# Kernel tuning notes

Measured on AMD Instinct MI355X. Metric: run time of the kernel, lower is better.

Reference implementation:

```python
import jax, jax.numpy as jnp
import numpy as np

N, D, K = 8192, 128, 128  # nodes, feature dim, clusters
E = 262144                # edges per graph


def mish(x):
    return x * jnp.tanh(jax.nn.softplus(x))


def sage(x, src, dst, Wl, bl, Wr):
    # PyG SAGEConv: mean-aggregate source features at targets, then lin_l(agg)+lin_r(x)
    agg = jax.ops.segment_sum(x[src], dst, num_segments=N)            # [N,D]
    cnt = jax.ops.segment_sum(jnp.ones((src.shape[0],), x.dtype), dst, num_segments=N)
    mean = agg / jnp.maximum(cnt, 1.0)[:, None]
    return mean @ Wl + bl + x @ Wr


def dmon(x, adj, W1, b1, W2, b2):
    # DMoNPooling (PyG): MLP -> softmax assignments, pooled feats, 3 losses.
    s = jax.nn.softmax((x @ W1 + b1) @ W2 + b2, axis=-1)              # [N,K]
    out = jax.nn.selu(s.T @ x)                                        # [K,D]
    out_adj = s.T @ adj @ s                                           # [K,K]
    deg = adj.sum(-1, keepdims=True)                                  # [N,1]
    m = deg.sum() / 2
    ca = s.T @ deg                                                    # [K,1]
    normalizer = (ca @ ca.T) / 2 / m
    spectral = -jnp.trace(out_adj - normalizer) / 2 / m
    ss = s.T @ s
    i_norm = jnp.sqrt(jnp.asarray(K, x.dtype))                        # ||I_K||_F
    ortho = jnp.linalg.norm(ss / jnp.linalg.norm(ss) - jnp.eye(K, dtype=x.dtype) / i_norm)
    cluster = jnp.linalg.norm(s.sum(0)) / N * i_norm - 1
    return out, spectral, ortho, cluster


def dense_adj(e):
    adj = jnp.zeros((N, N), jnp.float32)
    return adj.at[e[0], e[1]].add(1.0)


def setup_inputs():
    key = jax.random.key(0)
    ks = jax.random.split(key, 24)
    w = lambda k, shp: jax.random.normal(k, shp, jnp.float32) * 0.05
    inp = {
        'x1': jax.random.normal(ks[0], (N, D), jnp.float32),
        'x2': jax.random.normal(ks[1], (N, D), jnp.float32),
        'e1': jax.random.randint(ks[2], (2, E), 0, N),
        'e2': jax.random.randint(ks[3], (2, E), 0, N),
    }
    names = ['c1', 'c2', 'co', 'c3', 'c4']
    for i, nm in enumerate(names):
        inp[nm + '_Wl'] = w(ks[4 + 3 * i], (D, D))
        inp[nm + '_bl'] = jnp.zeros((D,), jnp.float32)
        inp[nm + '_Wr'] = w(ks[5 + 3 * i], (D, D))
    inp['m_W1'] = w(ks[20], (D, D))
    inp['m_b1'] = jnp.zeros((D,), jnp.float32)
    inp['m_W2'] = w(ks[21], (D, K))
    inp['m_b2'] = jnp.zeros((K,), jnp.float32)
    return inp


def reference(x1, x2, e1, e2,
              c1_Wl, c1_bl, c1_Wr, c2_Wl, c2_bl, c2_Wr,
              co_Wl, co_bl, co_Wr, c3_Wl, c3_bl, c3_Wr,
              c4_Wl, c4_bl, c4_Wr, m_W1, m_b1, m_W2, m_b2):
    s1, d1 = e1[0], e1[1]
    s2, d2 = e2[0], e2[1]
    h1 = mish(sage(x1, s1, d1, c1_Wl, c1_bl, c1_Wr))
    h2 = mish(sage(x2, s2, d2, c2_Wl, c2_bl, c2_Wr))
    co1 = mish(sage(h1, s1, d1, co_Wl, co_bl, co_Wr))
    co2 = mish(sage(h2, s2, d2, co_Wl, co_bl, co_Wr))
    h1 = mish(sage(h1 + co1, s1, d1, c3_Wl, c3_bl, c3_Wr))
    h2 = mish(sage(h2 + co2, s2, d2, c4_Wl, c4_bl, c4_Wr))
    p1, sp1, o1, cl1 = dmon(h1, dense_adj(e1), m_W1, m_b1, m_W2, m_b2)
    p2, sp2, o2, cl2 = dmon(h2, dense_adj(e2), m_W1, m_b1, m_W2, m_b2)
    x = jnp.concatenate([p1, p2], axis=0)[None]  # [1, 2K, D]
    return x, sp1 + o1 + cl1 + sp2 + o2 + cl2
```

## Files before the change

kernel.cpp:

```cpp
#include <hip/hip_runtime.h>
#include <math.h>

#define NN 8192
#define DD 128
#define KK 128
#define EE 262144
#define BCAP 128

typedef _Float16 f16;
typedef __attribute__((ext_vector_type(8))) _Float16 f16x8;
typedef __attribute__((ext_vector_type(4))) _Float16 f16x4;
typedef __attribute__((ext_vector_type(4))) float f32x4;

__device__ __forceinline__ float mishf(float v){
  float e  = __expf(v);
  float t2 = e * (e + 2.f);
  float r  = v * (t2 / (t2 + 2.f));
  return (v > 30.f) ? v : r;
}

__device__ __forceinline__ unsigned char enc_fp8(float f){
  unsigned u = __float_as_uint(f) + 0x00080000u;
  int e8 = (int)(u >> 23) - 120;
  if (e8 >= 1) return (unsigned char)(((unsigned)e8 << 3) | ((u >> 20) & 7u));
  return (unsigned char)(f * 512.f + 0.5f);
}
__device__ __forceinline__ float dec_fp8(unsigned b){
  unsigned e = (b >> 3) & 0xFu;
  return e ? __uint_as_float(((e + 120u) << 23) | ((b & 7u) << 20))
           : (float)(b & 7u) * 0.001953125f;
}

__global__ __launch_bounds__(256) void prep_kernel(
    const float* __restrict__ x0, const float* __restrict__ x1,
    f16* __restrict__ f0, f16* __restrict__ f1,
    const int* __restrict__ eA, const int* __restrict__ eB,
    int* cntA, int* degA, int* cntB, int* degB,
    int* __restrict__ bkA, int* __restrict__ bkB,
    const float* w0, const float* w1, const float* w2, const float* w3,
    const float* w4, const float* w5, const float* w6, const float* w7,
    const float* w8, const float* w9, const float* w10, const float* w11,
    f16* WT){
  int g = blockIdx.y;
  int bx = blockIdx.x;
  int t = threadIdx.x;
  if (bx < 512){
    const float* x = g ? x1 : x0;
    f16* f = g ? f1 : f0;
    int idx = bx * 256 + t;
    const float4* p = (const float4*)&x[idx * 8];
    float4 a = p[0], b = p[1];
    f16x8 o;
    o[0] = (f16)a.x; o[1] = (f16)a.y; o[2] = (f16)a.z; o[3] = (f16)a.w;
    o[4] = (f16)b.x; o[5] = (f16)b.y; o[6] = (f16)b.z; o[7] = (f16)b.w;
    *(f16x8*)&f[idx * 8] = o;
  } else if (bx < 768){
    const int* e  = g ? eB : eA;
    int* cnt = g ? cntB : cntA;
    int* deg = g ? degB : degA;
    int* bk  = g ? bkB  : bkA;
    const int* src = e;
    const int* dst = e + EE;
    for (int i = (bx - 512) * 256 + t; i < EE; i += 65536){
      int d = dst[i], s = src[i];
      int pos = atomicAdd(&cnt[d], 1);
      bk[d * BCAP + pos] = s;
      atomicAdd(&deg[s], 1);
    }
  } else {
    const float* Ws[12] = {w0,w1,w2,w3,w4,w5,w6,w7,w8,w9,w10,w11};
    int widx = (bx - 768) * 2 + g;
    const float* W = Ws[widx];
    f16* O = WT + (size_t)widx * 16384;
    int n = t >> 1, k0 = (t & 1) * 64;
#pragma unroll
    for (int seg = 0; seg < 8; ++seg){
      f16x8 o;
#pragma unroll
      for (int q = 0; q < 8; ++q)
        o[q] = (f16)W[(k0 + seg * 8 + q) * 128 + n];
      *(f16x8*)&O[n * 128 + k0 + seg * 8] = o;
    }
  }
}

template<int DUAL, int ACT, int FUSEADD>
__global__ __launch_bounds__(256) void aggemm(
    const int* __restrict__ cntA, const int* __restrict__ cntB,
    const int* __restrict__ bkA, const int* __restrict__ bkB,
    const f16* __restrict__ FA, const f16* __restrict__ FBg,
    const f16* __restrict__ BA, const f16* __restrict__ BBm,
    const f16* __restrict__ WaT0, const f16* __restrict__ WaT1,
    const f16* __restrict__ WbT0, const f16* __restrict__ WbT1,
    const float* __restrict__ bi0, const float* __restrict__ bi1,
    const f16* __restrict__ ADD0, const f16* __restrict__ ADD1,
    f16* __restrict__ O0, f16* __restrict__ O1){
  int g = blockIdx.y;
  const int* cnt = g ? cntB : cntA;
  const int* bk  = g ? bkB  : bkA;
  const f16* F  = g ? FBg : FA;
  const f16* Bm = g ? BBm : BA;
  const f16* WaT = g ? WaT1 : WaT0;
  const f16* WbT = g ? WbT1 : WbT0;
  const float* bi = g ? bi1 : bi0;
  const f16* ADD = g ? ADD1 : ADD0;
  f16* O = g ? O1 : O0;

  __shared__ f16 AT[32][136];
  int t = threadIdx.x;
  int rowBase = blockIdx.x * 32;

  {
    int r = t >> 3;
    int lane = t & 7;
    int c0 = lane * 16;
    int node = rowBase + r;
    int nc = cnt[node];
    const int* lst = bk + node * BCAP;
    float a[16];
#pragma unroll
    for (int k = 0; k < 16; ++k) a[k] = 0.f;
    int j = 0;
    for (; j + 4 <= nc; j += 4){
      int s0 = lst[j], s1 = lst[j + 1], s2 = lst[j + 2], s3 = lst[j + 3];
      f16x8 u0 = *(const f16x8*)&F[s0 * DD + c0];
      f16x8 u1 = *(const f16x8*)&F[s0 * DD + c0 + 8];
      f16x8 v0 = *(const f16x8*)&F[s1 * DD + c0];
      f16x8 v1 = *(const f16x8*)&F[s1 * DD + c0 + 8];
      f16x8 w0 = *(const f16x8*)&F[s2 * DD + c0];
      f16x8 w1 = *(const f16x8*)&F[s2 * DD + c0 + 8];
      f16x8 y0 = *(const f16x8*)&F[s3 * DD + c0];
      f16x8 y1 = *(const f16x8*)&F[s3 * DD + c0 + 8];
#pragma unroll
      for (int k = 0; k < 8; ++k){
        a[k]     += ((float)u0[k] + (float)v0[k]) + ((float)w0[k] + (float)y0[k]);
        a[k + 8] += ((float)u1[k] + (float)v1[k]) + ((float)w1[k] + (float)y1[k]);
      }
    }
    for (; j < nc; ++j){
      int s = lst[j];
      f16x8 u0 = *(const f16x8*)&F[s * DD + c0];
      f16x8 u1 = *(const f16x8*)&F[s * DD + c0 + 8];
#pragma unroll
      for (int k = 0; k < 8; ++k){ a[k] += (float)u0[k]; a[k + 8] += (float)u1[k]; }
    }
    float inv = 1.f / fmaxf((float)nc, 1.f);
    f16x8 o0, o1;
#pragma unroll
    for (int k = 0; k < 8; ++k){ o0[k] = (f16)(a[k] * inv); o1[k] = (f16)(a[k + 8] * inv); }
    *(f16x8*)&AT[r][c0]     = o0;
    *(f16x8*)&AT[r][c0 + 8] = o1;
  }
  __syncthreads();

  int wave = t >> 6, l = t & 63;
  int lrow = l & 15;
  int lk = (l >> 4) * 8;
  int rt = wave >> 1, nh = wave & 1;
  int rowW = rowBase + rt * 16;

  f32x4 acc[4];
#pragma unroll
  for (int q = 0; q < 4; ++q) acc[q] = (f32x4){0.f, 0.f, 0.f, 0.f};

#pragma unroll
  for (int kc = 0; kc < 4; ++kc){
    int kb = kc * 32 + lk;
    f16x8 a0 = *(const f16x8*)&AT[rt * 16 + lrow][kb];
#pragma unroll
    for (int q = 0; q < 4; ++q){
      int nt = nh * 4 + q;
      f16x8 bw = *(const f16x8*)&WaT[(nt * 16 + lrow) * 128 + kb];
      acc[q] = __builtin_amdgcn_mfma_f32_16x16x32_f16(a0, bw, acc[q], 0, 0, 0);
    }
    if (DUAL){
      f16x8 c0v = *(const f16x8*)&Bm[(rowW + lrow) * 128 + kb];
#pragma unroll
      for (int q = 0; q < 4; ++q){
        int nt = nh * 4 + q;
        f16x8 bw = *(const f16x8*)&WbT[(nt * 16 + lrow) * 128 + kb];
        acc[q] = __builtin_amdgcn_mfma_f32_16x16x32_f16(c0v, bw, acc[q], 0, 0, 0);
      }
    }
  }

  int col16 = l & 15;
  int rgrp = (l >> 4) * 4;
#pragma unroll
  for (int r = 0; r < 4; ++r){
    int row = rowW + rgrp + r;
    float v[4];
#pragma unroll
    for (int q = 0; q < 4; ++q) v[q] = acc[q][r] + bi[(nh * 4 + q) * 16 + col16];
    if (ACT == 1){
#pragma unroll
      for (int q = 0; q < 4; ++q) v[q] = mishf(v[q]);
    }
    if (FUSEADD){
#pragma unroll
      for (int q = 0; q < 4; ++q)
        v[q] += (float)ADD[row * 128 + (nh * 4 + q) * 16 + col16];
    }
#pragma unroll
    for (int q = 0; q < 4; ++q)
      O[row * 128 + (nh * 4 + q) * 16 + col16] = (f16)v[q];
  }
}

__global__ __launch_bounds__(128) void mlp_kernel(
    const f16* __restrict__ H0, const f16* __restrict__ H1,
    const f16* __restrict__ W1T, const f16* __restrict__ W2T,
    const float* __restrict__ b1, const float* __restrict__ b2,
    f16* __restrict__ O0, f16* __restrict__ O1,
    unsigned char* __restrict__ S80, unsigned char* __restrict__ S81){
  int g = blockIdx.y;
  const f16* A = g ? H1 : H0;
  f16* O = g ? O1 : O0;
  unsigned char* S8 = g ? S81 : S80;

  __shared__ f16 T[32][136];
  int t = threadIdx.x;
  int wave = t >> 6, l = t & 63;
  int lrow = l & 15;
  int lk = (l >> 4) * 8;
  int rowBase = blockIdx.x * 32 + wave * 16;
  int col16 = l & 15;
  int rgrp = (l >> 4) * 4;

  f32x4 acc[8];
#pragma unroll
  for (int nt = 0; nt < 8; ++nt) acc[nt] = (f32x4){0.f, 0.f, 0.f, 0.f};
#pragma unroll
  for (int kc = 0; kc < 4; ++kc){
    int kb = kc * 32 + lk;
    f16x8 a0 = *(const f16x8*)&A[(rowBase + lrow) * 128 + kb];
#pragma unroll
    for (int nt = 0; nt < 8; ++nt){
      f16x8 bw = *(const f16x8*)&W1T[(nt * 16 + lrow) * 128 + kb];
      acc[nt] = __builtin_amdgcn_mfma_f32_16x16x32_f16(a0, bw, acc[nt], 0, 0, 0);
    }
  }
#pragma unroll
  for (int r = 0; r < 4; ++r)
#pragma unroll
    for (int nt = 0; nt < 8; ++nt)
      T[wave * 16 + rgrp + r][nt * 16 + col16] = (f16)(acc[nt][r] + b1[nt * 16 + col16]);
  __syncthreads();

  f32x4 acc2[8];
#pragma unroll
  for (int nt = 0; nt < 8; ++nt) acc2[nt] = (f32x4){0.f, 0.f, 0.f, 0.f};
#pragma unroll
  for (int kc = 0; kc < 4; ++kc){
    int kb = kc * 32 + lk;
    f16x8 a0 = *(const f16x8*)&T[wave * 16 + lrow][kb];
#pragma unroll
    for (int nt = 0; nt < 8; ++nt){
      f16x8 bw = *(const f16x8*)&W2T[(nt * 16 + lrow) * 128 + kb];
      acc2[nt] = __builtin_amdgcn_mfma_f32_16x16x32_f16(a0, bw, acc2[nt], 0, 0, 0);
    }
  }

  float bv[8];
#pragma unroll
  for (int nt = 0; nt < 8; ++nt) bv[nt] = b2[nt * 16 + col16];
#pragma unroll
  for (int r = 0; r < 4; ++r){
    int row = rowBase + rgrp + r;
    float v[8];
#pragma unroll
    for (int nt = 0; nt < 8; ++nt) v[nt] = acc2[nt][r] + bv[nt];
    float m = v[0];
#pragma unroll
    for (int nt = 1; nt < 8; ++nt) m = fmaxf(m, v[nt]);
    for (int msk = 1; msk < 16; msk <<= 1) m = fmaxf(m, __shfl_xor(m, msk));
    float sum = 0.f;
#pragma unroll
    for (int nt = 0; nt < 8; ++nt){ v[nt] = __expf(v[nt] - m); sum += v[nt]; }
    for (int msk = 1; msk < 16; msk <<= 1) sum += __shfl_xor(sum, msk);
    float inv = 1.f / sum;
#pragma unroll
    for (int nt = 0; nt < 8; ++nt) v[nt] *= inv;
#pragma unroll
    for (int nt = 0; nt < 8; ++nt){
      O[row * 128 + nt * 16 + col16] = (f16)v[nt];
      S8[row * 128 + nt * 16 + col16] = enc_fp8(v[nt] * 64.f);
    }
  }
}

__global__ __launch_bounds__(256) void transpose_kernel(
    const f16* __restrict__ in0A, const f16* __restrict__ in1A,
    const f16* __restrict__ in0B, const f16* __restrict__ in1B,
    f16* __restrict__ o0A, f16* __restrict__ o1A,
    f16* __restrict__ o0B, f16* __restrict__ o1B,
    const int* __restrict__ dg0, const int* __restrict__ dg1,
    float* col0, float* col1, float* ca0, float* ca1){
  int g = blockIdx.y, z = blockIdx.z;
  const f16* in = z ? (g ? in1B : in0B) : (g ? in1A : in0A);
  f16* outp     = z ? (g ? o1B  : o0B)  : (g ? o1A  : o0A);
  __shared__ f16 T[32][136];
  int t = threadIdx.x;
  int i0 = blockIdx.x * 32;
#pragma unroll
  for (int j = 0; j < 2; ++j){
    int idx = t + j * 256;
    int row = idx >> 4, c8 = (idx & 15) * 8;
    f16x8 v = *(const f16x8*)&in[(i0 + row) * 128 + c8];
#pragma unroll
    for (int q = 0; q < 8; ++q) T[row][c8 + q] = v[q];
  }
  __syncthreads();
  int k = t >> 1, seg = (t & 1) * 16;
  f16x8 oA, oB;
#pragma unroll
  for (int q = 0; q < 8; ++q){ oA[q] = T[seg + q][k]; oB[q] = T[seg + 8 + q][k]; }
  *(f16x8*)&outp[(size_t)k * NN + i0 + seg]     = oA;
  *(f16x8*)&outp[(size_t)k * NN + i0 + seg + 8] = oB;

  if (z == 0){
    const int* dg = g ? dg1 : dg0;
    float* col = g ? col1 : col0;
    float* ca  = g ? ca1  : ca0;
    int kk = t & 127, half = t >> 7;
    float cs = 0.f, cc = 0.f;
#pragma unroll
    for (int i = 0; i < 16; ++i){
      int ri = half * 16 + i;
      float f = (float)T[ri][kk];
      cs += f;
      cc += f * (float)dg[i0 + ri];
    }
    atomicAdd(&col[kk], cs);
    atomicAdd(&ca[kk], cc);
  }
}

#define PK_NSPLIT 16
__global__ __launch_bounds__(256) void pooltrace_kernel(
    const f16* __restrict__ ST0, const f16* __restrict__ ST1,
    const f16* __restrict__ HT0, const f16* __restrict__ HT1,
    float* __restrict__ PART,
    const int* __restrict__ cntA, const int* __restrict__ cntB,
    const int* __restrict__ bkA, const int* __restrict__ bkB,
    const f16* __restrict__ SA, const f16* __restrict__ SBp,
    const unsigned char* __restrict__ S8A, const unsigned char* __restrict__ S8B,
    float* tr0, float* tr1){
  int g = blockIdx.y;
  int bx = blockIdx.x;
  int t = threadIdx.x;
  if (bx < 32){
    int z = bx >> 4, split = bx & 15;
    const f16* A = g ? ST1 : ST0;
    const f16* B = z ? A : (g ? HT1 : HT0);
    float* OUT = PART + ((size_t)(z * 2 + g) * PK_NSPLIT + split) * 16384;

    int wave = t >> 6, l = t & 63;
    int lrow = l & 15;
    int lk = (l >> 4) * 8;
    int krow = wave * 32;
    int i0 = split * (NN / PK_NSPLIT);

    f32x4 acc[2][8];
#pragma unroll
    for (int rt = 0; rt < 2; ++rt)
#pragma unroll
      for (int nt = 0; nt < 8; ++nt)
        acc[rt][nt] = (f32x4){0.f, 0.f, 0.f, 0.f};

#pragma unroll 2
    for (int c = 0; c < NN / PK_NSPLIT; c += 32){
      int ib = i0 + c + lk;
      f16x8 a0 = *(const f16x8*)&A[(size_t)(krow + lrow) * NN + ib];
      f16x8 a1 = *(const f16x8*)&A[(size_t)(krow + 16 + lrow) * NN + ib];
#pragma unroll
      for (int nt = 0; nt < 8; ++nt){
        f16x8 bf = *(const f16x8*)&B[(size_t)(nt * 16 + lrow) * NN + ib];
        acc[0][nt] = __builtin_amdgcn_mfma_f32_16x16x32_f16(a0, bf, acc[0][nt], 0, 0, 0);
        acc[1][nt] = __builtin_amdgcn_mfma_f32_16x16x32_f16(a1, bf, acc[1][nt], 0, 0, 0);
      }
    }

    int col = l & 15;
    int rbase = (l >> 4) * 4;
#pragma unroll
    for (int rt = 0; rt < 2; ++rt)
#pragma unroll
      for (int nt = 0; nt < 8; ++nt)
#pragma unroll
        for (int r = 0; r < 4; ++r)
          OUT[(krow + rt * 16 + rbase + r) * 128 + nt * 16 + col] = acc[rt][nt][r];
  } else {
    const int* cnt = g ? cntB : cntA;
    const int* bk  = g ? bkB  : bkA;
    const f16* S = g ? SBp : SA;
    const unsigned char* S8 = g ? S8B : S8A;
    float* tr = g ? tr1 : tr0;
    int grp = t >> 4, lane = t & 15;
    int node = (bx - 32) * 16 + grp;
    int nc = cnt[node];
    const int* lst = bk + node * BCAP;
    f16x8 w = *(const f16x8*)&S[node * DD + lane * 8];
    float o[8];
#pragma unroll
    for (int k = 0; k < 8; ++k) o[k] = (float)w[k];
    float acc = 0.f;
    int j = 0;
    for (; j + 4 <= nc; j += 4){
      int s0 = lst[j], s1 = lst[j + 1], s2 = lst[j + 2], s3 = lst[j + 3];
      uint2 q0 = *(const uint2*)&S8[s0 * DD + lane * 8];
      uint2 q1 = *(const uint2*)&S8[s1 * DD + lane * 8];
      uint2 q2 = *(const uint2*)&S8[s2 * DD + lane * 8];
      uint2 q3 = *(const uint2*)&S8[s3 * DD + lane * 8];
#pragma unroll
      for (int k = 0; k < 4; ++k){
        float lo = (dec_fp8((q0.x >> (8*k)) & 0xFF) + dec_fp8((q1.x >> (8*k)) & 0xFF))
                 + (dec_fp8((q2.x >> (8*k)) & 0xFF) + dec_fp8((q3.x >> (8*k)) & 0xFF));
        float hi = (dec_fp8((q0.y >> (8*k)) & 0xFF) + dec_fp8((q1.y >> (8*k)) & 0xFF))
                 + (dec_fp8((q2.y >> (8*k)) & 0xFF) + dec_fp8((q3.y >> (8*k)) & 0xFF));
        acc += o[k] * lo + o[k + 4] * hi;
      }
    }
    for (; j < nc; ++j){
      int s = lst[j];
      uint2 q = *(const uint2*)&S8[s * DD + lane * 8];
#pragma unroll
      for (int k = 0; k < 4; ++k){
        acc += o[k] * dec_fp8((q.x >> (8*k)) & 0xFF)
             + o[k + 4] * dec_fp8((q.y >> (8*k)) & 0xFF);
      }
    }
    for (int m = 1; m < 16; m <<= 1) acc += __shfl_xor(acc, m);
    __shared__ float part[16];
    if (lane == 0) part[grp] = acc;
    __syncthreads();
    if (t == 0){
      float s = 0.f;
#pragma unroll
      for (int i = 0; i < 16; ++i) s += part[i];
      atomicAdd(tr, s * 0.015625f);
    }
  }
}

__global__ __launch_bounds__(256) void reduce_kernel(
    const float* __restrict__ PART,
    float* __restrict__ out, float* F2acc, float* trssacc){
  int g = blockIdx.y, z = blockIdx.z;
  int t = threadIdx.x;
  int idx = blockIdx.x * 256 + t;
  const float* base = PART + (size_t)(z * 2 + g) * PK_NSPLIT * 16384 + idx;
  float s = 0.f;
#pragma unroll
  for (int sp = 0; sp < PK_NSPLIT; ++sp) s += base[sp * 16384];
  if (z == 0){
    const float scale = 1.0507009873554805f, alpha = 1.6732632423543772f;
    float r = (s > 0.f) ? scale * s : scale * alpha * expm1f(s);
    out[g * 16384 + idx] = r;
  } else {
    float f2p = s * s;
    float trp = (idx % 129 == 0) ? s : 0.f;
    __shared__ float r1[256], r2[256];
    r1[t] = f2p; r2[t] = trp; __syncthreads();
    for (int o = 128; o > 0; o >>= 1){
      if (t < o){ r1[t] += r1[t + o]; r2[t] += r2[t + o]; }
      __syncthreads();
    }
    if (t == 0){
      atomicAdd(&F2acc[g], r1[0]);
      atomicAdd(&trssacc[g], r2[0]);
    }
  }
}

__global__ __launch_bounds__(128) void finalize_kernel(
    const float* col0, const float* col1, const float* ca0, const float* ca1,
    const float* tr0, const float* tr1, const float* F2acc, const float* trssacc,
    float* loss_out){
  __shared__ float r1[128], r2[128];
  __shared__ float total_s;
  int t = threadIdx.x;
  if (t == 0) total_s = 0.f;
  for (int g = 0; g < 2; ++g){
    const float* col = g ? col1 : col0;
    const float* ca  = g ? ca1  : ca0;
    const float* tr  = g ? tr1  : tr0;
    __syncthreads();
    r1[t] = ca[t] * ca[t];
    r2[t] = col[t] * col[t];
    __syncthreads();
    for (int o = 64; o > 0; o >>= 1){
      if (t < o){ r1[t] += r1[t + o]; r2[t] += r2[t + o]; }
      __syncthreads();
    }
    if (t == 0){
      float ca2 = r1[0], cs2 = r2[0];
      float F = sqrtf(F2acc[g]);
      float ortho = sqrtf(fmaxf(2.f - 2.f * trssacc[g] / (F * sqrtf((float)KK)), 0.f));
      float m2 = (float)EE;
      float spectral = -(tr[0] - ca2 / m2) / m2;
      float cluster = sqrtf(cs2) / (float)NN * sqrtf((float)KK) - 1.f;
      total_s += spectral + ortho + cluster;
    }
  }
  __syncthreads();
  if (t == 0) loss_out[0] = total_s;
}

extern "C" void kernel_launch(void* const* d_in, const int* in_sizes, int n_in,
                              void* d_out, int out_size, void* d_ws, size_t ws_size,
                              hipStream_t stream){
  const float* x1 = (const float*)d_in[0];
  const float* x2 = (const float*)d_in[1];
  const int*   e1 = (const int*)d_in[2];
  const int*   e2 = (const int*)d_in[3];
  const float* c1_Wl = (const float*)d_in[4];
  const float* c1_bl = (const float*)d_in[5];
  const float* c1_Wr = (const float*)d_in[6];
  const float* c2_Wl = (const float*)d_in[7];
  const float* c2_bl = (const float*)d_in[8];
  const float* c2_Wr = (const float*)d_in[9];
  const float* co_Wl = (const float*)d_in[10];
  const float* co_bl = (const float*)d_in[11];
  const float* co_Wr = (const float*)d_in[12];
  const float* c3_Wl = (const float*)d_in[13];
  const float* c3_bl = (const float*)d_in[14];
  const float* c3_Wr = (const float*)d_in[15];
  const float* c4_Wl = (const float*)d_in[16];
  const float* c4_bl = (const float*)d_in[17];
  const float* c4_Wr = (const float*)d_in[18];
  const float* m_W1 = (const float*)d_in[19];
  const float* m_b1 = (const float*)d_in[20];
  const float* m_W2 = (const float*)d_in[21];
  const float* m_b2 = (const float*)d_in[22];
  float* out = (float*)d_out;

  char* w = (char*)d_ws;
  auto alloc = [&](size_t bytes) -> char* {
    char* p = w;
    w += (bytes + 255) / 256 * 256;
    return p;
  };
  int* cnt0 = (int*)alloc(NN * 4);
  int* deg0 = (int*)alloc(NN * 4);
  int* cnt1 = (int*)alloc(NN * 4);
  int* deg1 = (int*)alloc(NN * 4);
  float* col0 = (float*)alloc(128 * 4);
  float* ca0  = (float*)alloc(128 * 4);
  float* tr0  = (float*)alloc(256);
  float* col1 = (float*)alloc(128 * 4);
  float* ca1  = (float*)alloc(128 * 4);
  float* tr1  = (float*)alloc(256);
  float* F2acc   = (float*)alloc(2 * 4);
  float* trssacc = (float*)alloc(2 * 4);
  size_t zero_len = (size_t)(w - (char*)cnt0);
  int* bk0 = (int*)alloc((size_t)NN * BCAP * 4);
  int* bk1 = (int*)alloc((size_t)NN * BCAP * 4);
  float* PART = (float*)alloc((size_t)4 * PK_NSPLIT * 16384 * 4);
  f16* WT = (f16*)alloc(12 * 16384 * sizeof(f16));
  unsigned char* S8_0 = (unsigned char*)alloc((size_t)NN * DD);
  unsigned char* S8_1 = (unsigned char*)alloc((size_t)NN * DD);
  f16* F1_0 = (f16*)alloc((size_t)NN * DD * 2);
  f16* F3_0 = (f16*)alloc((size_t)NN * DD * 2);
  f16* F4_0 = (f16*)alloc((size_t)NN * DD * 2);
  f16* F5_0 = (f16*)alloc((size_t)NN * DD * 2);
  f16* F1_1 = (f16*)alloc((size_t)NN * DD * 2);
  f16* F3_1 = (f16*)alloc((size_t)NN * DD * 2);
  f16* F4_1 = (f16*)alloc((size_t)NN * DD * 2);
  f16* F5_1 = (f16*)alloc((size_t)NN * DD * 2);

  hipMemsetAsync(cnt0, 0, zero_len, stream);

  prep_kernel<<<dim3(774, 2), 256, 0, stream>>>(
      x1, x2, F1_0, F1_1, e1, e2, cnt0, deg0, cnt1, deg1, bk0, bk1,
      c1_Wl, c1_Wr, c2_Wl, c2_Wr, co_Wl, co_Wr,
      c3_Wl, c3_Wr, c4_Wl, c4_Wr, m_W1, m_W2, WT);

  f16* W_c1l = WT;            f16* W_c1r = WT + 16384;
  f16* W_c2l = WT + 2*16384;  f16* W_c2r = WT + 3*16384;
  f16* W_col = WT + 4*16384;  f16* W_cor = WT + 5*16384;
  f16* W_c3l = WT + 6*16384;  f16* W_c3r = WT + 7*16384;
  f16* W_c4l = WT + 8*16384;  f16* W_c4r = WT + 9*16384;
  f16* W_m1  = WT + 10*16384; f16* W_m2  = WT + 11*16384;

  aggemm<1, 1, 0><<<dim3(256, 2), 256, 0, stream>>>(cnt0, cnt1, bk0, bk1,
      F1_0, F1_1, F1_0, F1_1, W_c1l, W_c2l, W_c1r, W_c2r, c1_bl, c2_bl,
      nullptr, nullptr, F3_0, F3_1);

  aggemm<1, 1, 1><<<dim3(256, 2), 256, 0, stream>>>(cnt0, cnt1, bk0, bk1,
      F3_0, F3_1, F3_0, F3_1, W_col, W_col, W_cor, W_cor, co_bl, co_bl,
      F3_0, F3_1, F1_0, F1_1);

  aggemm<1, 1, 0><<<dim3(256, 2), 256, 0, stream>>>(cnt0, cnt1, bk0, bk1,
      F1_0, F1_1, F1_0, F1_1, W_c3l, W_c4l, W_c3r, W_c4r, c3_bl, c4_bl,
      nullptr, nullptr, F4_0, F4_1);

  mlp_kernel<<<dim3(256, 2), 128, 0, stream>>>(F4_0, F4_1, W_m1, W_m2,
      m_b1, m_b2, F5_0, F5_1, S8_0, S8_1);

  transpose_kernel<<<dim3(256, 2, 2), 256, 0, stream>>>(
      F5_0, F5_1, F4_0, F4_1, F1_0, F1_1, F3_0, F3_1,
      deg0, deg1, col0, col1, ca0, ca1);

  pooltrace_kernel<<<dim3(544, 2), 256, 0, stream>>>(
      F1_0, F1_1, F3_0, F3_1, PART,
      cnt0, cnt1, bk0, bk1, F5_0, F5_1, S8_0, S8_1, tr0, tr1);
  reduce_kernel<<<dim3(64, 2, 2), 256, 0, stream>>>(PART, out, F2acc, trssacc);

  finalize_kernel<<<1, 128, 0, stream>>>(col0, col1, ca0, ca1, tr0, tr1,
      F2acc, trssacc, out + 32768);
}
```

Baseline: 213.0 us.

## Compute degree-weighted assignment sums from edge lists instead of degree atomics

Removes the per-edge atomic degree histogram in prep and the degree-weighted column sum in transpose. ca = s^T deg is now accumulated during the edge-list trace pass by summing the decoded fp8 assignment rows of each node's neighbours, since sum_i s_i deg_i equals the sum over edges of s_src. The trace pass also splits each node's edge list into two halves across separate blocks, doubling the grid for more parallelism. This adds shared-memory reductions and 128 extra atomics per block, and ca now uses fp8-quantised assignments.

```diff
diff --git a/kernel.cpp b/kernel.cpp
--- a/kernel.cpp
+++ b/kernel.cpp
@@ -35,7 +35,7 @@
     const float* __restrict__ x0, const float* __restrict__ x1,
     f16* __restrict__ f0, f16* __restrict__ f1,
     const int* __restrict__ eA, const int* __restrict__ eB,
-    int* cntA, int* degA, int* cntB, int* degB,
+    int* cntA, int* cntB,
     int* __restrict__ bkA, int* __restrict__ bkB,
     const float* w0, const float* w1, const float* w2, const float* w3,
     const float* w4, const float* w5, const float* w6, const float* w7,
@@ -57,7 +57,6 @@
   } else if (bx < 768){
     const int* e  = g ? eB : eA;
     int* cnt = g ? cntB : cntA;
-    int* deg = g ? degB : degA;
     int* bk  = g ? bkB  : bkA;
     const int* src = e;
     const int* dst = e + EE;
@@ -65,7 +64,6 @@
       int d = dst[i], s = src[i];
       int pos = atomicAdd(&cnt[d], 1);
       bk[d * BCAP + pos] = s;
-      atomicAdd(&deg[s], 1);
     }
   } else {
     const float* Ws[12] = {w0,w1,w2,w3,w4,w5,w6,w7,w8,w9,w10,w11};
@@ -294,8 +292,7 @@
     const f16* __restrict__ in0B, const f16* __restrict__ in1B,
     f16* __restrict__ o0A, f16* __restrict__ o1A,
     f16* __restrict__ o0B, f16* __restrict__ o1B,
-    const int* __restrict__ dg0, const int* __restrict__ dg1,
-    float* col0, float* col1, float* ca0, float* ca1){
+    float* col0, float* col1){
   int g = blockIdx.y, z = blockIdx.z;
   const f16* in = z ? (g ? in1B : in0B) : (g ? in1A : in0A);
   f16* outp     = z ? (g ? o1B  : o0B)  : (g ? o1A  : o0A);
@@ -319,20 +316,13 @@
   *(f16x8*)&outp[(size_t)k * NN + i0 + seg + 8] = oB;
 
   if (z == 0){
-    const int* dg = g ? dg1 : dg0;
     float* col = g ? col1 : col0;
-    float* ca  = g ? ca1  : ca0;
     int kk = t & 127, half = t >> 7;
-    float cs = 0.f, cc = 0.f;
-#pragma unroll
-    for (int i = 0; i < 16; ++i){
-      int ri = half * 16 + i;
-      float f = (float)T[ri][kk];
-      cs += f;
-      cc += f * (float)dg[i0 + ri];
-    }
+    float cs = 0.f;
+#pragma unroll
+    for (int i = 0; i < 16; ++i)
+      cs += (float)T[half * 16 + i][kk];
     atomicAdd(&col[kk], cs);
-    atomicAdd(&ca[kk], cc);
   }
 }
 
@@ -345,7 +335,7 @@
     const int* __restrict__ bkA, const int* __restrict__ bkB,
     const f16* __restrict__ SA, const f16* __restrict__ SBp,
     const unsigned char* __restrict__ S8A, const unsigned char* __restrict__ S8B,
-    float* tr0, float* tr1){
+    float* tr0, float* tr1, float* ca0, float* ca1){
   int g = blockIdx.y;
   int bx = blockIdx.x;
   int t = threadIdx.x;
@@ -396,17 +386,22 @@
     const f16* S = g ? SBp : SA;
     const unsigned char* S8 = g ? S8B : S8A;
     float* tr = g ? tr1 : tr0;
+    float* ca = g ? ca1 : ca0;
     int grp = t >> 4, lane = t & 15;
-    int node = (bx - 32) * 16 + grp;
+    int bb = bx - 32;
+    int node = (bb >> 1) * 16 + grp;
+    int half = bb & 1;
     int nc = cnt[node];
+    int j0 = half ? (nc >> 1) : 0;
+    int j1 = half ? nc : (nc >> 1);
     const int* lst = bk + node * BCAP;
     f16x8 w = *(const f16x8*)&S[node * DD + lane * 8];
-    float o[8];
-#pragma unroll
-    for (int k = 0; k < 8; ++k) o[k] = (float)w[k];
+    float o[8], cak[8];
+#pragma unroll
+    for (int k = 0; k < 8; ++k){ o[k] = (float)w[k]; cak[k] = 0.f; }
     float acc = 0.f;
-    int j = 0;
-    for (; j + 4 <= nc; j += 4){
+    int j = j0;
+    for (; j + 4 <= j1; j += 4){
       int s0 = lst[j], s1 = lst[j + 1], s2 = lst[j + 2], s3 = lst[j + 3];
       uint2 q0 = *(const uint2*)&S8[s0 * DD + lane * 8];
       uint2 q1 = *(const uint2*)&S8[s1 * DD + lane * 8];
@@ -419,26 +414,38 @@
         float hi = (dec_fp8((q0.y >> (8*k)) & 0xFF) + dec_fp8((q1.y >> (8*k)) & 0xFF))
                  + (dec_fp8((q2.y >> (8*k)) & 0xFF) + dec_fp8((q3.y >> (8*k)) & 0xFF));
         acc += o[k] * lo + o[k + 4] * hi;
+        cak[k] += lo; cak[k + 4] += hi;
       }
     }
-    for (; j < nc; ++j){
+    for (; j < j1; ++j){
       int s = lst[j];
       uint2 q = *(const uint2*)&S8[s * DD + lane * 8];
 #pragma unroll
       for (int k = 0; k < 4; ++k){
-        acc += o[k] * dec_fp8((q.x >> (8*k)) & 0xFF)
-             + o[k + 4] * dec_fp8((q.y >> (8*k)) & 0xFF);
+        float lo = dec_fp8((q.x >> (8*k)) & 0xFF);
+        float hi = dec_fp8((q.y >> (8*k)) & 0xFF);
+        acc += o[k] * lo + o[k + 4] * hi;
+        cak[k] += lo; cak[k + 4] += hi;
       }
     }
     for (int m = 1; m < 16; m <<= 1) acc += __shfl_xor(acc, m);
     __shared__ float part[16];
+    __shared__ float pca[16][128];
     if (lane == 0) part[grp] = acc;
+#pragma unroll
+    for (int k = 0; k < 8; ++k) pca[grp][lane * 8 + k] = cak[k];
     __syncthreads();
     if (t == 0){
       float s = 0.f;
 #pragma unroll
       for (int i = 0; i < 16; ++i) s += part[i];
       atomicAdd(tr, s * 0.015625f);
+    }
+    if (t < 128){
+      float s = 0.f;
+#pragma unroll
+      for (int i = 0; i < 16; ++i) s += pca[i][t];
+      atomicAdd(&ca[t], s * 0.015625f);
     }
   }
 }
@@ -542,9 +549,7 @@
     return p;
   };
   int* cnt0 = (int*)alloc(NN * 4);
-  int* deg0 = (int*)alloc(NN * 4);
   int* cnt1 = (int*)alloc(NN * 4);
-  int* deg1 = (int*)alloc(NN * 4);
   float* col0 = (float*)alloc(128 * 4);
   float* ca0  = (float*)alloc(128 * 4);
   float* tr0  = (float*)alloc(256);
@@ -572,7 +577,7 @@
   hipMemsetAsync(cnt0, 0, zero_len, stream);
 
   prep_kernel<<<dim3(774, 2), 256, 0, stream>>>(
-      x1, x2, F1_0, F1_1, e1, e2, cnt0, deg0, cnt1, deg1, bk0, bk1,
+      x1, x2, F1_0, F1_1, e1, e2, cnt0, cnt1, bk0, bk1,
       c1_Wl, c1_Wr, c2_Wl, c2_Wr, co_Wl, co_Wr,
       c3_Wl, c3_Wr, c4_Wl, c4_Wr, m_W1, m_W2, WT);
 
@@ -599,12 +604,11 @@
       m_b1, m_b2, F5_0, F5_1, S8_0, S8_1);
 
   transpose_kernel<<<dim3(256, 2, 2), 256, 0, stream>>>(
-      F5_0, F5_1, F4_0, F4_1, F1_0, F1_1, F3_0, F3_1,
-      deg0, deg1, col0, col1, ca0, ca1);
-
-  pooltrace_kernel<<<dim3(544, 2), 256, 0, stream>>>(
+      F5_0, F5_1, F4_0, F4_1, F1_0, F1_1, F3_0, F3_1, col0, col1);
+
+  pooltrace_kernel<<<dim3(1056, 2), 256, 0, stream>>>(
       F1_0, F1_1, F3_0, F3_1, PART,
-      cnt0, cnt1, bk0, bk1, F5_0, F5_1, S8_0, S8_1, tr0, tr1);
+      cnt0, cnt1, bk0, bk1, F5_0, F5_1, S8_0, S8_1, tr0, tr1, ca0, ca1);
   reduce_kernel<<<dim3(64, 2, 2), 256, 0, stream>>>(PART, out, F2acc, trssacc);
 
   finalize_kernel<<<1, 128, 0, stream>>>(col0, col1, ca0, ca1, tr0, tr1,
```

After: 219.5 us. 1.03x slower.
